# Optimization experiments

Measured on AMD Instinct MI355X. Metric: run time of the kernel, lower is better.

The kernel has to match this reference:

```python
import jax, jax.numpy as jnp
import numpy as np

B, C, E, TARGET = 8, 256, 18000, 4500


def setup_inputs() -> dict:
    key = jax.random.key(0)
    k1, k2 = jax.random.split(key)
    fe = jax.random.normal(k1, (B, C, E), dtype=jnp.float32)
    # group_ids[b, e] = index of the pooled output edge that original edge e
    # was merged into by the union-find during edge collapse.
    group_ids = jax.random.randint(k2, (B, E), 0, TARGET, dtype=jnp.int64)
    return {"fe": fe, "group_ids": group_ids, "target": TARGET}


def reference(fe, group_ids, target):
    # MeshUnion.rebuild_features: out feature of each surviving edge group =
    # mean of features of all original edges merged into that group.
    b, c, e = fe.shape
    # flatten (batch, group) into one segment id so a single segment_sum handles all meshes
    flat_ids = (jnp.arange(b, dtype=group_ids.dtype)[:, None] * target + group_ids).reshape(-1)  # [B*E]
    feats = fe.transpose(0, 2, 1).reshape(b * e, c)  # [B*E, C]
    sums = jax.ops.segment_sum(feats, flat_ids, num_segments=b * target)          # [B*T, C]
    counts = jax.ops.segment_sum(jnp.ones((b * e,), fe.dtype), flat_ids,
                                 num_segments=b * target)                          # [B*T]
    out = sums / jnp.maximum(counts, 1.0)[:, None]
    return out.reshape(b, target, c).transpose(0, 2, 1)  # [B, C, target]
```

## Files before the change

kernel.cpp:

```cpp
#include <hip/hip_runtime.h>

#define BB 8
#define CC 256
#define EE 18000
#define TT 4500
#define BT (BB * TT)
#define BE (BB * EE)
#define NT 1024
#define W  18
#define PW (NT * W)


__global__ void zero_counts_kernel(int* __restrict__ counts) {
    int i = blockIdx.x * blockDim.x + threadIdx.x;
    if (i < BT) counts[i] = 0;
}

__global__ void count_kernel(const int* __restrict__ gid, int* __restrict__ counts) {
    int i = blockIdx.x * blockDim.x + threadIdx.x;
    if (i < BE) {
        int b = i / EE;
        atomicAdd(&counts[b * TT + gid[i]], 1);
    }
}

__global__ __launch_bounds__(1024) void scan_kernel(const int* __restrict__ counts,
                                                    int* __restrict__ cursor,
                                                    uint2* __restrict__ tab) {
    __shared__ int part[1024];
    const int b = blockIdx.x;
    const int t = threadIdx.x;
    const int CHUNK = 5;
    int lo = t * CHUNK; if (lo > TT) lo = TT;
    int hi = lo + CHUNK; if (hi > TT) hi = TT;
    int s = 0;
    for (int i = lo; i < hi; ++i) s += counts[b * TT + i];
    part[t] = s;
    __syncthreads();
    for (int d = 1; d < 1024; d <<= 1) {
        int v = (t >= d) ? part[t - d] : 0;
        __syncthreads();
        part[t] += v;
        __syncthreads();
    }
    int run = part[t] - s;
    for (int i = lo; i < hi; ++i) {
        int cnt = counts[b * TT + i];
        cursor[b * TT + i] = b * EE + run;
        int en = run + cnt;
        float inv = cnt ? 1.0f / (float)cnt : 0.0f;
        tab[b * TT + i] = make_uint2((unsigned)run | ((unsigned)en << 16),
                                     __float_as_uint(inv));
        run = en;
    }
}

__global__ void scatter_kernel(const int* __restrict__ gid,
                               int* __restrict__ cursor,
                               unsigned short* __restrict__ prank16) {
    int i = blockIdx.x * blockDim.x + threadIdx.x;
    if (i < BE) {
        int b = i / EE;
        int p = atomicAdd(&cursor[b * TT + gid[i]], 1) - b * EE;
        prank16[i] = (unsigned short)p;
    }
}


__global__ __launch_bounds__(1024, 8) void pool_kernel(const float* __restrict__ fe,
                                                       const unsigned short* __restrict__ prank16,
                                                       const uint2* __restrict__ tab,
                                                       float* __restrict__ out) {
    __shared__ float vals[PW];
    __shared__ float wsum[16];
    const int b   = blockIdx.x >> 8;
    const int c   = blockIdx.x & 255;
    const int tid = threadIdx.x;
    const int wv  = tid >> 6;
    const int ln  = tid & 63;

    const float4*  fe4 = (const float4*)(fe + (size_t)(b * CC + c) * EE);
    const ushort4* rk4 = (const ushort4*)(prank16 + (size_t)b * EE);
#pragma unroll
    for (int i = 0; i < 5; ++i) {
        int idx = tid + (i << 10);
        if (idx < EE / 4) {
            float4  v = fe4[idx];
            ushort4 r = rk4[idx];
            vals[r.x] = v.x;
            vals[r.y] = v.y;
            vals[r.z] = v.z;
            vals[r.w] = v.w;
        }
    }
    __syncthreads();

    const int base = W * tid;
    float2 pv[9];
    float  csum[9];
#pragma unroll
    for (int k = 0; k < 9; ++k) {
        float2 v = *reinterpret_cast<const float2*>(&vals[base + (k << 1)]);
        float p0 = v.x;
        float p1 = p0 + v.y;
        pv[k] = make_float2(p0, p1);
        csum[k] = p1;
    }
    float t01 = csum[0] + csum[1], t23 = csum[2] + csum[3];
    float t45 = csum[4] + csum[5], t67 = csum[6] + csum[7];
    const float sum = ((t01 + t23) + (t45 + t67)) + csum[8];

    float sc = sum;
#pragma unroll
    for (int d = 1; d < 64; d <<= 1) {
        float o = __shfl_up(sc, d, 64);
        if (ln >= d) sc += o;
    }
    if (ln == 63) wsum[wv] = sc;
    __syncthreads();

    float cross = 0.0f;
#pragma unroll
    for (int j = 0; j < 16; ++j) {
        float tw = wsum[j];
        if (j < wv) cross += tw;
    }

    float off = cross + (sc - sum);
#pragma unroll
    for (int k = 0; k < 9; ++k) {
        float2 p = pv[k];
        *reinterpret_cast<float2*>(&vals[base + (k << 1)]) =
            make_float2(p.x + off, p.y + off);
        off += csum[k];
    }
    __syncthreads();

    const uint2* tbB  = tab + b * TT;
    float*       outb = out + (size_t)(b * CC + c) * TT;
    for (int s = tid; s < TT / 4; s += NT) {
        const uint2* tb = tbB + (s << 2);
        uint4 qA = *reinterpret_cast<const uint4*>(tb);
        uint4 qB = *reinterpret_cast<const uint4*>(tb + 2);

        unsigned se0 = qA.x, se1 = qA.z, se2 = qB.x, se3 = qB.z;
        float iv0 = __uint_as_float(qA.y), iv1 = __uint_as_float(qA.w);
        float iv2 = __uint_as_float(qB.y), iv3 = __uint_as_float(qB.w);

        unsigned st0 = se0 & 0xffffu;
        unsigned en0 = se0 >> 16, en1 = se1 >> 16, en2 = se2 >> 16, en3 = se3 >> 16;

        float Pp = vals[(st0 ? st0 : 1u) - 1u]; Pp = st0 ? Pp : 0.0f;
        float P0 = vals[(en0 ? en0 : 1u) - 1u]; P0 = en0 ? P0 : 0.0f;
        float P1 = vals[(en1 ? en1 : 1u) - 1u]; P1 = en1 ? P1 : 0.0f;
        float P2 = vals[(en2 ? en2 : 1u) - 1u]; P2 = en2 ? P2 : 0.0f;
        float P3 = vals[(en3 ? en3 : 1u) - 1u]; P3 = en3 ? P3 : 0.0f;

        float4 o;
        o.x = (P0 - Pp) * iv0;
        o.y = (P1 - P0) * iv1;
        o.z = (P2 - P1) * iv2;
        o.w = (P3 - P2) * iv3;

        *reinterpret_cast<float4*>(outb + (s << 2)) = o;
    }
}

extern "C" void kernel_launch(void* const* d_in, const int* in_sizes, int n_in,
                              void* d_out, int out_size, void* d_ws, size_t ws_size,
                              hipStream_t stream) {
    const float* fe  = (const float*)d_in[0];
    const int*   gid = (const int*)d_in[1];
    float*       out = (float*)d_out;

    int*            counts  = (int*)d_ws;
    int*            cursor  = counts + BT;
    uint2*          tab     = (uint2*)(cursor + BT);
    unsigned short* prank16 = (unsigned short*)(tab + BT);

    zero_counts_kernel<<<(BT + 255) / 256, 256, 0, stream>>>(counts);
    count_kernel<<<(BE + 255) / 256, 256, 0, stream>>>(gid, counts);
    scan_kernel<<<BB, 1024, 0, stream>>>(counts, cursor, tab);
    scatter_kernel<<<(BE + 255) / 256, 256, 0, stream>>>(gid, cursor, prank16);
    pool_kernel<<<BB * CC, 1024, 0, stream>>>(fe, prank16, tab, out);
}
```

Before: 62.80 us.

## Process two channels per block in pool kernel with float2 shared scan

Each pool block now handles a pair of channels, storing interleaved float2 values in shared memory and running the prefix scan and segment-difference gather for both at once. This amortizes the rank and table loads, index math and block synchronization over two channels and halves the grid. It doubles shared memory per block to about 147 KB, so fewer blocks can be resident per CU and latency hiding may suffer.

```diff
diff --git a/kernel.cpp b/kernel.cpp
--- a/kernel.cpp
+++ b/kernel.cpp
@@ -67,77 +67,87 @@
 }
 
 
-__global__ __launch_bounds__(1024, 8) void pool_kernel(const float* __restrict__ fe,
+__global__ __launch_bounds__(1024, 4) void pool_kernel(const float* __restrict__ fe,
                                                        const unsigned short* __restrict__ prank16,
                                                        const uint2* __restrict__ tab,
                                                        float* __restrict__ out) {
-    __shared__ float vals[PW];
-    __shared__ float wsum[16];
-    const int b   = blockIdx.x >> 8;
-    const int c   = blockIdx.x & 255;
+    __shared__ float2 vals2[PW];
+    __shared__ float2 wsum[16];
+    const int b   = blockIdx.x >> 7;
+    const int cp  = blockIdx.x & 127;
+    const int c0  = cp << 1;
     const int tid = threadIdx.x;
     const int wv  = tid >> 6;
     const int ln  = tid & 63;
 
-    const float4*  fe4 = (const float4*)(fe + (size_t)(b * CC + c) * EE);
+    const float4*  feA = (const float4*)(fe + (size_t)(b * CC + c0) * EE);
+    const float4*  feB = (const float4*)(fe + (size_t)(b * CC + c0 + 1) * EE);
     const ushort4* rk4 = (const ushort4*)(prank16 + (size_t)b * EE);
 #pragma unroll
     for (int i = 0; i < 5; ++i) {
         int idx = tid + (i << 10);
         if (idx < EE / 4) {
-            float4  v = fe4[idx];
-            ushort4 r = rk4[idx];
-            vals[r.x] = v.x;
-            vals[r.y] = v.y;
-            vals[r.z] = v.z;
-            vals[r.w] = v.w;
+            float4  va = feA[idx];
+            float4  vb = feB[idx];
+            ushort4 r  = rk4[idx];
+            vals2[r.x] = make_float2(va.x, vb.x);
+            vals2[r.y] = make_float2(va.y, vb.y);
+            vals2[r.z] = make_float2(va.z, vb.z);
+            vals2[r.w] = make_float2(va.w, vb.w);
         }
     }
     __syncthreads();
 
     const int base = W * tid;
-    float2 pv[9];
-    float  csum[9];
+    float4 pv[9];
+    float2 csum[9];
 #pragma unroll
     for (int k = 0; k < 9; ++k) {
-        float2 v = *reinterpret_cast<const float2*>(&vals[base + (k << 1)]);
-        float p0 = v.x;
-        float p1 = p0 + v.y;
-        pv[k] = make_float2(p0, p1);
-        csum[k] = p1;
+        float4 v = *reinterpret_cast<const float4*>(&vals2[base + (k << 1)]);
+        float q1x = v.x + v.z;
+        float q1y = v.y + v.w;
+        pv[k] = make_float4(v.x, v.y, q1x, q1y);
+        csum[k] = make_float2(q1x, q1y);
     }
-    float t01 = csum[0] + csum[1], t23 = csum[2] + csum[3];
-    float t45 = csum[4] + csum[5], t67 = csum[6] + csum[7];
-    const float sum = ((t01 + t23) + (t45 + t67)) + csum[8];
+    float2 t01 = make_float2(csum[0].x + csum[1].x, csum[0].y + csum[1].y);
+    float2 t23 = make_float2(csum[2].x + csum[3].x, csum[2].y + csum[3].y);
+    float2 t45 = make_float2(csum[4].x + csum[5].x, csum[4].y + csum[5].y);
+    float2 t67 = make_float2(csum[6].x + csum[7].x, csum[6].y + csum[7].y);
+    const float sumx = ((t01.x + t23.x) + (t45.x + t67.x)) + csum[8].x;
+    const float sumy = ((t01.y + t23.y) + (t45.y + t67.y)) + csum[8].y;
 
-    float sc = sum;
+    float scx = sumx, scy = sumy;
 #pragma unroll
     for (int d = 1; d < 64; d <<= 1) {
-        float o = __shfl_up(sc, d, 64);
-        if (ln >= d) sc += o;
+        float ox = __shfl_up(scx, d, 64);
+        float oy = __shfl_up(scy, d, 64);
+        if (ln >= d) { scx += ox; scy += oy; }
     }
-    if (ln == 63) wsum[wv] = sc;
+    if (ln == 63) wsum[wv] = make_float2(scx, scy);
     __syncthreads();
 
-    float cross = 0.0f;
+    float crx = 0.0f, cry = 0.0f;
 #pragma unroll
     for (int j = 0; j < 16; ++j) {
-        float tw = wsum[j];
-        if (j < wv) cross += tw;
+        float2 tw = wsum[j];
+        if (j < wv) { crx += tw.x; cry += tw.y; }
     }
 
-    float off = cross + (sc - sum);
+    float offx = crx + (scx - sumx);
+    float offy = cry + (scy - sumy);
 #pragma unroll
     for (int k = 0; k < 9; ++k) {
-        float2 p = pv[k];
-        *reinterpret_cast<float2*>(&vals[base + (k << 1)]) =
-            make_float2(p.x + off, p.y + off);
-        off += csum[k];
+        float4 p = pv[k];
+        *reinterpret_cast<float4*>(&vals2[base + (k << 1)]) =
+            make_float4(p.x + offx, p.y + offy, p.z + offx, p.w + offy);
+        offx += csum[k].x;
+        offy += csum[k].y;
     }
     __syncthreads();
 
-    const uint2* tbB  = tab + b * TT;
-    float*       outb = out + (size_t)(b * CC + c) * TT;
+    const uint2* tbB   = tab + b * TT;
+    float*       outb0 = out + (size_t)(b * CC + c0) * TT;
+    float*       outb1 = outb0 + TT;
     for (int s = tid; s < TT / 4; s += NT) {
         const uint2* tb = tbB + (s << 2);
         uint4 qA = *reinterpret_cast<const uint4*>(tb);
@@ -150,19 +160,20 @@
         unsigned st0 = se0 & 0xffffu;
         unsigned en0 = se0 >> 16, en1 = se1 >> 16, en2 = se2 >> 16, en3 = se3 >> 16;
 
-        float Pp = vals[(st0 ? st0 : 1u) - 1u]; Pp = st0 ? Pp : 0.0f;
-        float P0 = vals[(en0 ? en0 : 1u) - 1u]; P0 = en0 ? P0 : 0.0f;
-        float P1 = vals[(en1 ? en1 : 1u) - 1u]; P1 = en1 ? P1 : 0.0f;
-        float P2 = vals[(en2 ? en2 : 1u) - 1u]; P2 = en2 ? P2 : 0.0f;
-        float P3 = vals[(en3 ? en3 : 1u) - 1u]; P3 = en3 ? P3 : 0.0f;
+        float2 Pp = vals2[(st0 ? st0 : 1u) - 1u]; if (!st0) Pp = make_float2(0.f, 0.f);
+        float2 P0 = vals2[(en0 ? en0 : 1u) - 1u]; if (!en0) P0 = make_float2(0.f, 0.f);
+        float2 P1 = vals2[(en1 ? en1 : 1u) - 1u]; if (!en1) P1 = make_float2(0.f, 0.f);
+        float2 P2 = vals2[(en2 ? en2 : 1u) - 1u]; if (!en2) P2 = make_float2(0.f, 0.f);
+        float2 P3 = vals2[(en3 ? en3 : 1u) - 1u]; if (!en3) P3 = make_float2(0.f, 0.f);
 
-        float4 o;
-        o.x = (P0 - Pp) * iv0;
-        o.y = (P1 - P0) * iv1;
-        o.z = (P2 - P1) * iv2;
-        o.w = (P3 - P2) * iv3;
+        float4 o0, o1;
+        o0.x = (P0.x - Pp.x) * iv0;  o1.x = (P0.y - Pp.y) * iv0;
+        o0.y = (P1.x - P0.x) * iv1;  o1.y = (P1.y - P0.y) * iv1;
+        o0.z = (P2.x - P1.x) * iv2;  o1.z = (P2.y - P1.y) * iv2;
+        o0.w = (P3.x - P2.x) * iv3;  o1.w = (P3.y - P2.y) * iv3;
 
-        *reinterpret_cast<float4*>(outb + (s << 2)) = o;
+        *reinterpret_cast<float4*>(outb0 + (s << 2)) = o0;
+        *reinterpret_cast<float4*>(outb1 + (s << 2)) = o1;
     }
 }
 
@@ -182,5 +193,5 @@
     count_kernel<<<(BE + 255) / 256, 256, 0, stream>>>(gid, counts);
     scan_kernel<<<BB, 1024, 0, stream>>>(counts, cursor, tab);
     scatter_kernel<<<(BE + 255) / 256, 256, 0, stream>>>(gid, cursor, prank16);
-    pool_kernel<<<BB * CC, 1024, 0, stream>>>(fe, prank16, tab, out);
+    pool_kernel<<<BB * (CC / 2), 1024, 0, stream>>>(fe, prank16, tab, out);
 }
```

Result: slower. 75.23 us (+19.8%).

## Compact group-end prefix sums into output-indexed slots and precompute scatter ranks

Applied to the files above, without the earlier changes.

In the pool kernel, the in-place prefix-sum writeback to shared memory is replaced by writes only at group-end positions, compacted into slots indexed by group id. Each output then reads a contiguous float4 of group-end sums plus one gathered value for the previous group's end. The count kernel now records each edge's rank within its group, so the scatter stage no longer needs a second round of atomics. The scan uses a wave-shuffle scan with fewer threads, a new table kernel is added, and zeroing switches to hipMemsetAsync. This trades an extra small kernel and a larger workspace for fewer shared-memory stores and gathers in the main pool kernel.

```diff
diff --git a/kernel.cpp b/kernel.cpp
--- a/kernel.cpp
+++ b/kernel.cpp
@@ -7,61 +7,87 @@
 #define BT (BB * TT)
 #define BE (BB * EE)
 #define NT 1024
-#define W  18
-#define PW (NT * W)
-
-
-__global__ void zero_counts_kernel(int* __restrict__ counts) {
-    int i = blockIdx.x * blockDim.x + threadIdx.x;
-    if (i < BT) counts[i] = 0;
-}
-
-__global__ void count_kernel(const int* __restrict__ gid, int* __restrict__ counts) {
+#define GT (9 * 1024)
+
+
+__global__ void count_kernel(const int* __restrict__ gid,
+                             int* __restrict__ counts,
+                             unsigned short* __restrict__ rkin16) {
     int i = blockIdx.x * blockDim.x + threadIdx.x;
     if (i < BE) {
         int b = i / EE;
-        atomicAdd(&counts[b * TT + gid[i]], 1);
-    }
-}
-
-__global__ __launch_bounds__(1024) void scan_kernel(const int* __restrict__ counts,
-                                                    int* __restrict__ cursor,
-                                                    uint2* __restrict__ tab) {
-    __shared__ int part[1024];
-    const int b = blockIdx.x;
-    const int t = threadIdx.x;
-    const int CHUNK = 5;
-    int lo = t * CHUNK; if (lo > TT) lo = TT;
-    int hi = lo + CHUNK; if (hi > TT) hi = TT;
+        int rk = atomicAdd(&counts[b * TT + gid[i]], 1);
+        rkin16[i] = (unsigned short)rk;
+    }
+}
+
+__global__ __launch_bounds__(256) void scan_kernel(const int* __restrict__ counts,
+                                                   int* __restrict__ off32,
+                                                   unsigned short* __restrict__ gidx16,
+                                                   unsigned short* __restrict__ gidxT16) {
+    __shared__ int wsum[4];
+    const int b  = blockIdx.x;
+    const int t  = threadIdx.x;
+    const int wv = t >> 6;
+    const int ln = t & 63;
+    const int lo = t * 18;
+
     int s = 0;
-    for (int i = lo; i < hi; ++i) s += counts[b * TT + i];
-    part[t] = s;
-    __syncthreads();
-    for (int d = 1; d < 1024; d <<= 1) {
-        int v = (t >= d) ? part[t - d] : 0;
-        __syncthreads();
-        part[t] += v;
-        __syncthreads();
-    }
-    int run = part[t] - s;
-    for (int i = lo; i < hi; ++i) {
-        int cnt = counts[b * TT + i];
-        cursor[b * TT + i] = b * EE + run;
-        int en = run + cnt;
-        float inv = cnt ? 1.0f / (float)cnt : 0.0f;
-        tab[b * TT + i] = make_uint2((unsigned)run | ((unsigned)en << 16),
-                                     __float_as_uint(inv));
-        run = en;
+    if (lo < TT) {
+        for (int j = 0; j < 18; ++j) s += counts[b * TT + lo + j];
+    }
+    int sc = s;
+    for (int d = 1; d < 64; d <<= 1) {
+        int o = __shfl_up(sc, d, 64);
+        if (ln >= d) sc += o;
+    }
+    if (ln == 63) wsum[wv] = sc;
+    __syncthreads();
+    int cross = 0;
+    for (int j = 0; j < 4; ++j) { int w = wsum[j]; if (j < wv) cross += w; }
+
+    if (lo < TT) {
+        int run = cross + (sc - s);
+        for (int j = 0; j < 18; ++j) {
+            int g   = lo + j;
+            int cnt = counts[b * TT + g];
+            off32[b * TT + g] = run;
+            int en = run + cnt;
+            if (cnt) {
+                int ep = en - 1;
+                gidx16[b * EE + ep] = (unsigned short)g;
+                int wt = ep / 18, k = ep % 18;
+                gidxT16[((b * 9 + (k >> 1)) * 1024 + wt) * 2 + (k & 1)] =
+                    (unsigned short)(0x8000u | (unsigned)g);
+            }
+            run = en;
+        }
+    }
+}
+
+__global__ void table_kernel(const int* __restrict__ counts,
+                             const int* __restrict__ off32,
+                             const unsigned short* __restrict__ gidx16,
+                             uint2* __restrict__ tabJ) {
+    int i = blockIdx.x * blockDim.x + threadIdx.x;
+    if (i < BT) {
+        int b   = i / TT;
+        int st  = off32[i];
+        int cnt = counts[i];
+        unsigned jp  = st ? (unsigned)gidx16[b * EE + st - 1] : 0xFFFFu;
+        float    inv = cnt ? 1.0f / (float)cnt : 0.0f;
+        tabJ[i] = make_uint2(jp, __float_as_uint(inv));
     }
 }
 
 __global__ void scatter_kernel(const int* __restrict__ gid,
-                               int* __restrict__ cursor,
+                               const int* __restrict__ off32,
+                               const unsigned short* __restrict__ rkin16,
                                unsigned short* __restrict__ prank16) {
     int i = blockIdx.x * blockDim.x + threadIdx.x;
     if (i < BE) {
         int b = i / EE;
-        int p = atomicAdd(&cursor[b * TT + gid[i]], 1) - b * EE;
+        int p = off32[b * TT + gid[i]] + (int)rkin16[i];
         prank16[i] = (unsigned short)p;
     }
 }
@@ -69,9 +95,10 @@
 
 __global__ __launch_bounds__(1024, 8) void pool_kernel(const float* __restrict__ fe,
                                                        const unsigned short* __restrict__ prank16,
-                                                       const uint2* __restrict__ tab,
+                                                       const unsigned int* __restrict__ gidxT32,
+                                                       const uint2* __restrict__ tabJ,
                                                        float* __restrict__ out) {
-    __shared__ float vals[PW];
+    __shared__ float vals[NT * 18];
     __shared__ float wsum[16];
     const int b   = blockIdx.x >> 8;
     const int c   = blockIdx.x & 255;
@@ -95,20 +122,17 @@
     }
     __syncthreads();
 
-    const int base = W * tid;
+    const float2* smem2 = reinterpret_cast<const float2*>(vals);
+    const int fbase = 9 * tid;
     float2 pv[9];
-    float  csum[9];
 #pragma unroll
     for (int k = 0; k < 9; ++k) {
-        float2 v = *reinterpret_cast<const float2*>(&vals[base + (k << 1)]);
-        float p0 = v.x;
-        float p1 = p0 + v.y;
-        pv[k] = make_float2(p0, p1);
-        csum[k] = p1;
-    }
-    float t01 = csum[0] + csum[1], t23 = csum[2] + csum[3];
-    float t45 = csum[4] + csum[5], t67 = csum[6] + csum[7];
-    const float sum = ((t01 + t23) + (t45 + t67)) + csum[8];
+        float2 v = smem2[fbase + k];
+        pv[k] = make_float2(v.x, v.x + v.y);
+    }
+    float t01 = pv[0].y + pv[1].y, t23 = pv[2].y + pv[3].y;
+    float t45 = pv[4].y + pv[5].y, t67 = pv[6].y + pv[7].y;
+    const float sum = ((t01 + t23) + (t45 + t67)) + pv[8].y;
 
     float sc = sum;
 #pragma unroll
@@ -126,43 +150,38 @@
         if (j < wv) cross += tw;
     }
 
-    float off = cross + (sc - sum);
+    const unsigned int* gxT = gidxT32 + b * GT;
+    float run = cross + (sc - sum);
 #pragma unroll
     for (int k = 0; k < 9; ++k) {
-        float2 p = pv[k];
-        *reinterpret_cast<float2*>(&vals[base + (k << 1)]) =
-            make_float2(p.x + off, p.y + off);
-        off += csum[k];
-    }
-    __syncthreads();
-
-    const uint2* tbB  = tab + b * TT;
+        unsigned w = gxT[(k << 10) + tid];
+        if (w & 0x8000u)     vals[w & 0x7fffu]         = run + pv[k].x;
+        if (w & 0x80000000u) vals[(w >> 16) & 0x7fffu] = run + pv[k].y;
+        run += pv[k].y;
+    }
+    __syncthreads();
+
+    const uint2* tb   = tabJ + b * TT;
     float*       outb = out + (size_t)(b * CC + c) * TT;
     for (int s = tid; s < TT / 4; s += NT) {
-        const uint2* tb = tbB + (s << 2);
-        uint4 qA = *reinterpret_cast<const uint4*>(tb);
-        uint4 qB = *reinterpret_cast<const uint4*>(tb + 2);
-
-        unsigned se0 = qA.x, se1 = qA.z, se2 = qB.x, se3 = qB.z;
+        int base4 = s << 2;
+        uint4 qA = *reinterpret_cast<const uint4*>(tb + base4);
+        uint4 qB = *reinterpret_cast<const uint4*>(tb + base4 + 2);
+
+        float4 Cv = *reinterpret_cast<const float4*>(&vals[base4]);
+        float B0 = (qA.x != 0xFFFFu) ? vals[qA.x] : 0.0f;
+        float B1 = (qA.z != 0xFFFFu) ? vals[qA.z] : 0.0f;
+        float B2 = (qB.x != 0xFFFFu) ? vals[qB.x] : 0.0f;
+        float B3 = (qB.z != 0xFFFFu) ? vals[qB.z] : 0.0f;
         float iv0 = __uint_as_float(qA.y), iv1 = __uint_as_float(qA.w);
         float iv2 = __uint_as_float(qB.y), iv3 = __uint_as_float(qB.w);
 
-        unsigned st0 = se0 & 0xffffu;
-        unsigned en0 = se0 >> 16, en1 = se1 >> 16, en2 = se2 >> 16, en3 = se3 >> 16;
-
-        float Pp = vals[(st0 ? st0 : 1u) - 1u]; Pp = st0 ? Pp : 0.0f;
-        float P0 = vals[(en0 ? en0 : 1u) - 1u]; P0 = en0 ? P0 : 0.0f;
-        float P1 = vals[(en1 ? en1 : 1u) - 1u]; P1 = en1 ? P1 : 0.0f;
-        float P2 = vals[(en2 ? en2 : 1u) - 1u]; P2 = en2 ? P2 : 0.0f;
-        float P3 = vals[(en3 ? en3 : 1u) - 1u]; P3 = en3 ? P3 : 0.0f;
-
         float4 o;
-        o.x = (P0 - Pp) * iv0;
-        o.y = (P1 - P0) * iv1;
-        o.z = (P2 - P1) * iv2;
-        o.w = (P3 - P2) * iv3;
-
-        *reinterpret_cast<float4*>(outb + (s << 2)) = o;
+        o.x = (Cv.x - B0) * iv0;
+        o.y = (Cv.y - B1) * iv1;
+        o.z = (Cv.z - B2) * iv2;
+        o.w = (Cv.w - B3) * iv3;
+        *reinterpret_cast<float4*>(outb + base4) = o;
     }
 }
 
@@ -174,13 +193,18 @@
     float*       out = (float*)d_out;
 
     int*            counts  = (int*)d_ws;
-    int*            cursor  = counts + BT;
-    uint2*          tab     = (uint2*)(cursor + BT);
-    unsigned short* prank16 = (unsigned short*)(tab + BT);
-
-    zero_counts_kernel<<<(BT + 255) / 256, 256, 0, stream>>>(counts);
-    count_kernel<<<(BE + 255) / 256, 256, 0, stream>>>(gid, counts);
-    scan_kernel<<<BB, 1024, 0, stream>>>(counts, cursor, tab);
-    scatter_kernel<<<(BE + 255) / 256, 256, 0, stream>>>(gid, cursor, prank16);
-    pool_kernel<<<BB * CC, 1024, 0, stream>>>(fe, prank16, tab, out);
-}
+    unsigned int*   gidxT32 = (unsigned int*)(counts + BT);
+    int*            off32   = (int*)(gidxT32 + BB * GT);
+    uint2*          tabJ    = (uint2*)(off32 + BT);
+    unsigned short* gidx16  = (unsigned short*)(tabJ + BT);
+    unsigned short* rkin16  = gidx16 + (size_t)BB * EE;
+    unsigned short* prank16 = rkin16 + BE;
+
+    hipMemsetAsync(d_ws, 0, (size_t)(BT + BB * GT) * 4, stream);
+    count_kernel<<<(BE + 255) / 256, 256, 0, stream>>>(gid, counts, rkin16);
+    scan_kernel<<<BB, 256, 0, stream>>>(counts, off32, gidx16,
+                                        (unsigned short*)gidxT32);
+    table_kernel<<<(BT + 255) / 256, 256, 0, stream>>>(counts, off32, gidx16, tabJ);
+    scatter_kernel<<<(BE + 255) / 256, 256, 0, stream>>>(gid, off32, rkin16, prank16);
+    pool_kernel<<<BB * CC, 1024, 0, stream>>>(fe, prank16, gidxT32, tabJ, out);
+}
```

Measured after the change: 74.92 us. 1.19x slower.

## Reuse count-atomic ranks to drop scatter atomics and use wave-shuffle scan

Applied to the files above, without the earlier changes.

The count kernel now stores the value returned by its atomicAdd as each edge's rank within its group. The scatter pass then computes the final position as group offset plus that rank, with no second round of atomics. The per-batch scan moves from a 1024-thread shared-memory Hillis-Steele scan to 256 threads with 18 items each and wave shuffles. The pool kernel also issues all of its global loads before doing the LDS scatter. The cost is an extra 16-bit rank buffer, and the pool change may raise register pressure.

```diff
diff --git a/kernel.cpp b/kernel.cpp
--- a/kernel.cpp
+++ b/kernel.cpp
@@ -16,53 +16,68 @@
     if (i < BT) counts[i] = 0;
 }
 
-__global__ void count_kernel(const int* __restrict__ gid, int* __restrict__ counts) {
+__global__ void count_kernel(const int* __restrict__ gid,
+                             int* __restrict__ counts,
+                             unsigned short* __restrict__ rkin16) {
     int i = blockIdx.x * blockDim.x + threadIdx.x;
     if (i < BE) {
         int b = i / EE;
-        atomicAdd(&counts[b * TT + gid[i]], 1);
-    }
-}
-
-__global__ __launch_bounds__(1024) void scan_kernel(const int* __restrict__ counts,
-                                                    int* __restrict__ cursor,
-                                                    uint2* __restrict__ tab) {
-    __shared__ int part[1024];
-    const int b = blockIdx.x;
-    const int t = threadIdx.x;
-    const int CHUNK = 5;
-    int lo = t * CHUNK; if (lo > TT) lo = TT;
-    int hi = lo + CHUNK; if (hi > TT) hi = TT;
+        int rk = atomicAdd(&counts[b * TT + gid[i]], 1);
+        rkin16[i] = (unsigned short)rk;
+    }
+}
+
+__global__ __launch_bounds__(256) void scan_kernel(const int* __restrict__ counts,
+                                                   int* __restrict__ off32,
+                                                   uint2* __restrict__ tab) {
+    __shared__ int wtot[4];
+    const int b  = blockIdx.x;
+    const int t  = threadIdx.x;
+    const int wv = t >> 6;
+    const int ln = t & 63;
+    const int lo = t * W;
+
+    int cnt[W];
     int s = 0;
-    for (int i = lo; i < hi; ++i) s += counts[b * TT + i];
-    part[t] = s;
-    __syncthreads();
-    for (int d = 1; d < 1024; d <<= 1) {
-        int v = (t >= d) ? part[t - d] : 0;
-        __syncthreads();
-        part[t] += v;
-        __syncthreads();
-    }
-    int run = part[t] - s;
-    for (int i = lo; i < hi; ++i) {
-        int cnt = counts[b * TT + i];
-        cursor[b * TT + i] = b * EE + run;
-        int en = run + cnt;
-        float inv = cnt ? 1.0f / (float)cnt : 0.0f;
-        tab[b * TT + i] = make_uint2((unsigned)run | ((unsigned)en << 16),
-                                     __float_as_uint(inv));
-        run = en;
+    if (lo < TT) {
+#pragma unroll
+        for (int j = 0; j < W; ++j) { cnt[j] = counts[b * TT + lo + j]; s += cnt[j]; }
+    }
+    int sc = s;
+#pragma unroll
+    for (int d = 1; d < 64; d <<= 1) {
+        int o = __shfl_up(sc, d, 64);
+        if (ln >= d) sc += o;
+    }
+    if (ln == 63) wtot[wv] = sc;
+    __syncthreads();
+    int cross = 0;
+#pragma unroll
+    for (int j = 0; j < 4; ++j) { int w = wtot[j]; if (j < wv) cross += w; }
+
+    if (lo < TT) {
+        int run = cross + (sc - s);
+#pragma unroll
+        for (int j = 0; j < W; ++j) {
+            int g  = lo + j;
+            int en = run + cnt[j];
+            float inv = cnt[j] ? 1.0f / (float)cnt[j] : 0.0f;
+            off32[b * TT + g] = run;
+            tab[b * TT + g]   = make_uint2((unsigned)run | ((unsigned)en << 16),
+                                           __float_as_uint(inv));
+            run = en;
+        }
     }
 }
 
 __global__ void scatter_kernel(const int* __restrict__ gid,
-                               int* __restrict__ cursor,
+                               const int* __restrict__ off32,
+                               const unsigned short* __restrict__ rkin16,
                                unsigned short* __restrict__ prank16) {
     int i = blockIdx.x * blockDim.x + threadIdx.x;
     if (i < BE) {
         int b = i / EE;
-        int p = atomicAdd(&cursor[b * TT + gid[i]], 1) - b * EE;
-        prank16[i] = (unsigned short)p;
+        prank16[i] = (unsigned short)(off32[b * TT + gid[i]] + (int)rkin16[i]);
     }
 }
 
@@ -81,34 +96,39 @@
 
     const float4*  fe4 = (const float4*)(fe + (size_t)(b * CC + c) * EE);
     const ushort4* rk4 = (const ushort4*)(prank16 + (size_t)b * EE);
+    float4  v[5];
+    ushort4 r[5];
 #pragma unroll
     for (int i = 0; i < 5; ++i) {
         int idx = tid + (i << 10);
         if (idx < EE / 4) {
-            float4  v = fe4[idx];
-            ushort4 r = rk4[idx];
-            vals[r.x] = v.x;
-            vals[r.y] = v.y;
-            vals[r.z] = v.z;
-            vals[r.w] = v.w;
+            v[i] = fe4[idx];
+            r[i] = rk4[idx];
         }
     }
-    __syncthreads();
-
-    const int base = W * tid;
+#pragma unroll
+    for (int i = 0; i < 5; ++i) {
+        int idx = tid + (i << 10);
+        if (idx < EE / 4) {
+            vals[r[i].x] = v[i].x;
+            vals[r[i].y] = v[i].y;
+            vals[r[i].z] = v[i].z;
+            vals[r[i].w] = v[i].w;
+        }
+    }
+    __syncthreads();
+
+    const float2* smem2 = reinterpret_cast<const float2*>(vals);
+    const int fbase = 9 * tid;
     float2 pv[9];
-    float  csum[9];
 #pragma unroll
     for (int k = 0; k < 9; ++k) {
-        float2 v = *reinterpret_cast<const float2*>(&vals[base + (k << 1)]);
-        float p0 = v.x;
-        float p1 = p0 + v.y;
-        pv[k] = make_float2(p0, p1);
-        csum[k] = p1;
-    }
-    float t01 = csum[0] + csum[1], t23 = csum[2] + csum[3];
-    float t45 = csum[4] + csum[5], t67 = csum[6] + csum[7];
-    const float sum = ((t01 + t23) + (t45 + t67)) + csum[8];
+        float2 vv = smem2[fbase + k];
+        pv[k] = make_float2(vv.x, vv.x + vv.y);
+    }
+    float t01 = pv[0].y + pv[1].y, t23 = pv[2].y + pv[3].y;
+    float t45 = pv[4].y + pv[5].y, t67 = pv[6].y + pv[7].y;
+    const float sum = ((t01 + t23) + (t45 + t67)) + pv[8].y;
 
     float sc = sum;
 #pragma unroll
@@ -126,13 +146,13 @@
         if (j < wv) cross += tw;
     }
 
+    float2* smem2w = reinterpret_cast<float2*>(vals);
     float off = cross + (sc - sum);
 #pragma unroll
     for (int k = 0; k < 9; ++k) {
         float2 p = pv[k];
-        *reinterpret_cast<float2*>(&vals[base + (k << 1)]) =
-            make_float2(p.x + off, p.y + off);
-        off += csum[k];
+        smem2w[fbase + k] = make_float2(p.x + off, p.y + off);
+        off += p.y;
     }
     __syncthreads();
 
@@ -174,13 +194,14 @@
     float*       out = (float*)d_out;
 
     int*            counts  = (int*)d_ws;
-    int*            cursor  = counts + BT;
-    uint2*          tab     = (uint2*)(cursor + BT);
-    unsigned short* prank16 = (unsigned short*)(tab + BT);
+    int*            off32   = counts + BT;
+    uint2*          tab     = (uint2*)(off32 + BT);
+    unsigned short* rkin16  = (unsigned short*)(tab + BT);
+    unsigned short* prank16 = rkin16 + BE;
 
     zero_counts_kernel<<<(BT + 255) / 256, 256, 0, stream>>>(counts);
-    count_kernel<<<(BE + 255) / 256, 256, 0, stream>>>(gid, counts);
-    scan_kernel<<<BB, 1024, 0, stream>>>(counts, cursor, tab);
-    scatter_kernel<<<(BE + 255) / 256, 256, 0, stream>>>(gid, cursor, prank16);
+    count_kernel<<<(BE + 255) / 256, 256, 0, stream>>>(gid, counts, rkin16);
+    scan_kernel<<<BB, 256, 0, stream>>>(counts, off32, tab);
+    scatter_kernel<<<(BE + 255) / 256, 256, 0, stream>>>(gid, off32, rkin16, prank16);
     pool_kernel<<<BB * CC, 1024, 0, stream>>>(fe, prank16, tab, out);
 }
```

Result: faster. 58.45 us (-6.9%).
